# Performance work log

Measured on AMD Instinct MI355X. Metric: run time of the kernel, lower is better.

## Reference

```python
import jax, jax.numpy as jnp
import numpy as np

D_MODEL = 1024
N_STATE = 64
BASEWIDTH = 3
BC_SCALE = (D_MODEL / BASEWIDTH) ** -0.5  # 'mup' mode width_mult**-0.5
RMS_EPS = 1.1920928955078125e-07  # torch.finfo(float32).eps (RMSNorm eps=None default)


def setup_inputs() -> dict:
    key = jax.random.key(0)
    k1, k2, k3, k4 = jax.random.split(key, 4)
    Bsz, L = 4, 2048
    u = jax.random.normal(k1, (Bsz, D_MODEL, L), dtype=jnp.float32)
    A = jax.random.uniform(k2, (N_STATE,), dtype=jnp.float32) * 0.1  # buffer: rand(N)*A_scale
    B = (jax.random.normal(k3, (N_STATE, D_MODEL), dtype=jnp.float32) + 0.1) * BC_SCALE
    C = (jax.random.normal(k4, (N_STATE, D_MODEL), dtype=jnp.float32) + 0.1) * BC_SCALE
    D = jnp.ones((D_MODEL,), dtype=jnp.float32)
    norm_w = jnp.ones((D_MODEL,), dtype=jnp.float32)
    return {"L": L, "u": u, "A": A, "B": B, "C": C, "D": D, "norm_w": norm_w}


def _ssm(u, A, B, C, D, norm_w):
    # u: [b, d, l]
    scale = BC_SCALE  # applied to Bu, Cu in 'mup' hyperparam mode
    Bu = jnp.einsum('nd,bdl->bnl', B, u) * scale  # [b, n, l]
    Cu = jnp.einsum('nd,bdl->bnl', C, u) * scale  # [b, n, l]
    b, d, l = u.shape
    # shifted_delta == 1 (delta path commented out in source), so
    # h_{t} = A * h_{t-1} + Bu[:, :, t] (outer) u[:, :, t]
    h0 = jnp.zeros((b, d, A.shape[0]), dtype=u.dtype)

    def step(h, xs):
        bu_t, cu_t, u_t = xs  # [b,n], [b,n], [b,d]
        h = h * A + u_t[:, :, None] * bu_t[:, None, :]  # [b, d, n]
        y_t = jnp.einsum('bn,bdn->bd', cu_t, h)
        return h, y_t

    xs = (jnp.moveaxis(Bu, 2, 0), jnp.moveaxis(Cu, 2, 0), jnp.moveaxis(u, 2, 0))
    _, y = jax.lax.scan(step, h0, xs)  # y: [l, b, d]
    y = jnp.moveaxis(y, 0, 2).transpose(1, 0, 2) if False else jnp.transpose(y, (1, 2, 0))  # [b, d, l]
    out = y + u * D[None, :, None]
    # RMSNorm over d_model (apply in [b, l, d] layout)
    x = jnp.transpose(out, (0, 2, 1))  # [b, l, d]
    ms = jnp.mean(x * x, axis=-1, keepdims=True)
    x = x * jax.lax.rsqrt(ms + RMS_EPS) * norm_w
    return jnp.transpose(x, (0, 2, 1))  # [b, d, l]


def reference(L, u, A, B, C, D, norm_w):
    del L  # sequence length == u.shape[-1]
    return _ssm(u, A, B, C, D, norm_w)
```

## Files before the change

### kernel.cpp

```cpp
#include <hip/hip_runtime.h>
#include <stdint.h>

#define DM 1024
#define LS 2048
#define RMS_EPS 1.1920928955078125e-07f
#define S2 0.0029296875f

typedef __attribute__((ext_vector_type(8))) short bf16x8;
typedef __attribute__((ext_vector_type(4))) float f32x4;

__device__ __forceinline__ unsigned short f2bf(float f) {
  uint32_t u = __builtin_bit_cast(uint32_t, f);
  u += 0x7FFFu + ((u >> 16) & 1u);
  return (unsigned short)(u >> 16);
}

__global__ __launch_bounds__(256) void k0_prep(const float* __restrict__ B,
                                               const float* __restrict__ C,
                                               unsigned short* __restrict__ Bbf) {
  int i4 = blockIdx.x * 256 + threadIdx.x;
  const float4* src = (i4 < 16384) ? (const float4*)B : (const float4*)C;
  float4 v = src[i4 & 16383];
  ushort4 o;
  o.x = f2bf(v.x); o.y = f2bf(v.y); o.z = f2bf(v.z); o.w = f2bf(v.w);
  ((ushort4*)Bbf)[i4] = o;
}

__global__ __launch_bounds__(256) void k1_gemm(const float* __restrict__ u,
                                               const unsigned short* __restrict__ Bbf,
                                               float* __restrict__ BuCuT) {
  const int b    = blockIdx.y;
  const int l0   = blockIdx.x * 16;
  const int lane = threadIdx.x & 63;
  const int w    = threadIdx.x >> 6;
  const float* ub = u + (size_t)b * DM * LS;

  __shared__ bf16x8 tile[128][16];

  {
    const int lq = lane & 3;
    const int kg = lane >> 2;
    const int kbase = 256 * w + 16 * kg;
    #pragma unroll
    for (int h = 0; h < 2; ++h) {
      float4 vv[8];
      #pragma unroll
      for (int r = 0; r < 8; ++r)
        vv[r] = *(const float4*)(ub + (size_t)(kbase + 8*h + r) * LS + l0 + 4*lq);
      const int k8 = 32*w + 2*kg + h;
      #pragma unroll
      for (int c = 0; c < 4; ++c) {
        union { bf16x8 v; unsigned short s[8]; } t;
        #pragma unroll
        for (int r = 0; r < 8; ++r) t.s[r] = f2bf(((const float*)&vv[r])[c]);
        tile[k8][(4*lq + c) ^ (k8 & 3)] = t.v;
      }
    }
  }
  __syncthreads();

  const int n = lane & 15;
  const int q = lane >> 4;
  f32x4 acc[2] = {};
  #pragma unroll 4
  for (int it = 0; it < 32; ++it) {
    bf16x8 bfrag = tile[4*it + q][n ^ q];
    #pragma unroll
    for (int rt = 0; rt < 2; ++rt) {
      int row = 32*w + 16*rt + n;
      bf16x8 a = *(const bf16x8*)(Bbf + (size_t)row * DM + 32*it + 8*q);
      acc[rt] = __builtin_amdgcn_mfma_f32_16x16x32_bf16(a, bfrag, acc[rt], 0, 0, 0);
    }
  }

  float* ob = BuCuT + (size_t)b * LS * 128;
  #pragma unroll
  for (int rt = 0; rt < 2; ++rt) {
    int col = l0 + n;
    int row = 32*w + 16*rt + 4*q;
    *(f32x4*)(ob + (size_t)col * 128 + row) = acc[rt];
  }
}

__global__ __launch_bounds__(256) void k2_kw(const float* __restrict__ BuCuT,
                                             const float* __restrict__ A,
                                             float* __restrict__ Kw) {
  const int b  = blockIdx.y;
  const int t0 = blockIdx.x * 64;
  const int tl = threadIdx.x >> 2;
  const int p  = threadIdx.x & 3;
  const int t  = t0 + tl;
  const float* base = BuCuT + (size_t)b * LS * 128;

  float pw[16], aa[16];
  #pragma unroll
  for (int i = 0; i < 4; ++i) {
    float4 c4 = *(const float4*)(base + (size_t)t * 128 + 64 + 16*p + 4*i);
    float4 a4 = *(const float4*)(A + 16*p + 4*i);
    pw[4*i+0] = c4.x * S2; aa[4*i+0] = a4.x;
    pw[4*i+1] = c4.y * S2; aa[4*i+1] = a4.y;
    pw[4*i+2] = c4.z * S2; aa[4*i+2] = a4.z;
    pw[4*i+3] = c4.w * S2; aa[4*i+3] = a4.w;
  }
  float part[16];
  #pragma unroll
  for (int j = 0; j < 16; ++j) {
    float s = 0.f;
    if (t - j >= 0) {
      const float* bu = base + (size_t)(t - j) * 128 + 16*p;
      #pragma unroll
      for (int i = 0; i < 16; i += 4) {
        float4 b4 = *(const float4*)(bu + i);
        s = fmaf(pw[i+0], b4.x, s); s = fmaf(pw[i+1], b4.y, s);
        s = fmaf(pw[i+2], b4.z, s); s = fmaf(pw[i+3], b4.w, s);
      }
    }
    part[j] = s;
    #pragma unroll
    for (int i = 0; i < 16; ++i) pw[i] *= aa[i];
  }
  __shared__ float ss[64][68];
  #pragma unroll
  for (int j = 0; j < 16; ++j) ss[tl][p*17 + j] = part[j];
  __syncthreads();
  const int o  = threadIdx.x * 4;
  const int t2 = o >> 4;
  const int j0 = o & 15;
  float4 r;
  r.x = ss[t2][j0+0] + ss[t2][17+j0+0] + ss[t2][34+j0+0] + ss[t2][51+j0+0];
  r.y = ss[t2][j0+1] + ss[t2][17+j0+1] + ss[t2][34+j0+1] + ss[t2][51+j0+1];
  r.z = ss[t2][j0+2] + ss[t2][17+j0+2] + ss[t2][34+j0+2] + ss[t2][51+j0+2];
  r.w = ss[t2][j0+3] + ss[t2][17+j0+3] + ss[t2][34+j0+3] + ss[t2][51+j0+3];
  *(float4*)(Kw + ((size_t)b * LS + t0 + t2) * 16 + j0) = r;
}

__global__ __launch_bounds__(256) void k3_conv(const float* __restrict__ u,
                                               const float* __restrict__ Kw,
                                               const float* __restrict__ Dv,
                                               const float* __restrict__ nw,
                                               float* __restrict__ out) {
  const int b  = blockIdx.y;
  const int t0 = blockIdx.x * 16;
  const int tg = threadIdx.x & 3;
  const int dr = threadIdx.x >> 2;
  const float* ub = u + (size_t)b * DM * LS;
  float* ob = out + (size_t)b * DM * LS;

  float kw[4][16];
  #pragma unroll
  for (int k = 0; k < 4; ++k) {
    const float* kp = Kw + ((size_t)b * LS + t0 + 4*tg + k) * 16;
    #pragma unroll
    for (int i = 0; i < 4; ++i) {
      float4 v = *(const float4*)(kp + 4*i);
      kw[k][4*i+0] = v.x; kw[k][4*i+1] = v.y; kw[k][4*i+2] = v.z; kw[k][4*i+3] = v.w;
    }
  }

  const int cbase = t0 - 16 + 4*tg;
  float y[16][4];
  float ps[4] = {0.f, 0.f, 0.f, 0.f};
  #pragma unroll
  for (int c = 0; c < 16; ++c) {
    const int d = dr + 64*c;
    const float* row = ub + (size_t)d * LS;
    float wr[20];
    #pragma unroll
    for (int s5 = 0; s5 < 5; ++s5) {
      int g = cbase + 4*s5;
      float4 v;
      if (g >= 0) v = *(const float4*)(row + g);
      else        v = make_float4(0.f, 0.f, 0.f, 0.f);
      wr[4*s5+0] = v.x; wr[4*s5+1] = v.y; wr[4*s5+2] = v.z; wr[4*s5+3] = v.w;
    }
    const float Dd = Dv[d];
    #pragma unroll
    for (int k = 0; k < 4; ++k) {
      float acc = wr[16+k] * Dd;
      #pragma unroll
      for (int j = 0; j < 16; ++j)
        acc = fmaf(kw[k][j], wr[16 + k - j], acc);
      y[c][k] = acc;
      ps[k] = fmaf(acc, acc, ps[k]);
    }
  }

  __shared__ float ss[16][68];
  #pragma unroll
  for (int k = 0; k < 4; ++k) ss[4*tg + k][dr] = ps[k];
  __syncthreads();
  __shared__ float rsq[16];
  if (threadIdx.x < 16) {
    float s = 0.f;
    #pragma unroll
    for (int i = 0; i < 16; ++i) {
      float4 v = *(const float4*)&ss[threadIdx.x][4*i];
      s += (v.x + v.y) + (v.z + v.w);
    }
    rsq[threadIdx.x] = rsqrtf(s * (1.f/1024.f) + RMS_EPS);
  }
  __syncthreads();
  float rq[4];
  #pragma unroll
  for (int k = 0; k < 4; ++k) rq[k] = rsq[4*tg + k];
  #pragma unroll
  for (int c = 0; c < 16; ++c) {
    const int d = dr + 64*c;
    const float wn = nw[d];
    float4 o;
    o.x = y[c][0] * rq[0] * wn;
    o.y = y[c][1] * rq[1] * wn;
    o.z = y[c][2] * rq[2] * wn;
    o.w = y[c][3] * rq[3] * wn;
    *(float4*)(ob + (size_t)d * LS + t0 + 4*tg) = o;
  }
}

extern "C" void kernel_launch(void* const* d_in, const int* in_sizes, int n_in,
                              void* d_out, int out_size, void* d_ws, size_t ws_size,
                              hipStream_t stream) {
  const float* u  = (const float*)d_in[1];
  const float* A  = (const float*)d_in[2];
  const float* B  = (const float*)d_in[3];
  const float* C  = (const float*)d_in[4];
  const float* Dv = (const float*)d_in[5];
  const float* nw = (const float*)d_in[6];
  float* out = (float*)d_out;

  float* BuCuT = (float*)d_ws;
  float* Kw    = (float*)((char*)d_ws + (4u << 20));
  unsigned short* Bbf = (unsigned short*)((char*)d_ws + (4u << 20) + (512u << 10));

  k0_prep<<<dim3(128),    dim3(256), 0, stream>>>(B, C, Bbf);
  k1_gemm<<<dim3(128, 4), dim3(256), 0, stream>>>(u, Bbf, BuCuT);
  k2_kw  <<<dim3(32, 4),  dim3(256), 0, stream>>>(BuCuT, A, Kw);
  k3_conv<<<dim3(128, 4), dim3(256), 0, stream>>>(u, Kw, Dv, nw, out);
}
```

Before: 155.5 us.

## Pack conv kernel weights to bf16 and widen conv blocks to 512 threads

The per-timestep convolution weights written by k2 are now stored as packed bf16 pairs, which halves their footprint and the registers k3 needs to hold them. k3 moves to 512-thread blocks with 8 channel rows per thread instead of 16, cutting the per-thread y array in half to raise occupancy. k2 is reshaped to 128-thread blocks with twice as many blocks to spread work over more CUs. Rounding the kernel weights to bf16 adds precision loss to the output.

```diff
diff --git a/kernel.cpp b/kernel.cpp
--- a/kernel.cpp
+++ b/kernel.cpp
@@ -82,11 +82,11 @@
   }
 }
 
-__global__ __launch_bounds__(256) void k2_kw(const float* __restrict__ BuCuT,
+__global__ __launch_bounds__(128) void k2_kw(const float* __restrict__ BuCuT,
                                              const float* __restrict__ A,
-                                             float* __restrict__ Kw) {
+                                             uint32_t* __restrict__ Kwp) {
   const int b  = blockIdx.y;
-  const int t0 = blockIdx.x * 64;
+  const int t0 = blockIdx.x * 32;
   const int tl = threadIdx.x >> 2;
   const int p  = threadIdx.x & 3;
   const int t  = t0 + tl;
@@ -119,7 +119,7 @@
     #pragma unroll
     for (int i = 0; i < 16; ++i) pw[i] *= aa[i];
   }
-  __shared__ float ss[64][68];
+  __shared__ float ss[32][68];
   #pragma unroll
   for (int j = 0; j < 16; ++j) ss[tl][p*17 + j] = part[j];
   __syncthreads();
@@ -131,14 +131,17 @@
   r.y = ss[t2][j0+1] + ss[t2][17+j0+1] + ss[t2][34+j0+1] + ss[t2][51+j0+1];
   r.z = ss[t2][j0+2] + ss[t2][17+j0+2] + ss[t2][34+j0+2] + ss[t2][51+j0+2];
   r.w = ss[t2][j0+3] + ss[t2][17+j0+3] + ss[t2][34+j0+3] + ss[t2][51+j0+3];
-  *(float4*)(Kw + ((size_t)b * LS + t0 + t2) * 16 + j0) = r;
-}
-
-__global__ __launch_bounds__(256) void k3_conv(const float* __restrict__ u,
-                                               const float* __restrict__ Kw,
-                                               const float* __restrict__ Dv,
-                                               const float* __restrict__ nw,
-                                               float* __restrict__ out) {
+  uint2 pp;
+  pp.x = (uint32_t)f2bf(r.x) | ((uint32_t)f2bf(r.y) << 16);
+  pp.y = (uint32_t)f2bf(r.z) | ((uint32_t)f2bf(r.w) << 16);
+  *(uint2*)(Kwp + ((size_t)b * LS + t0 + t2) * 8 + (j0 >> 1)) = pp;
+}
+
+__global__ __launch_bounds__(512, 4) void k3_conv(const float* __restrict__ u,
+                                                  const uint32_t* __restrict__ Kwp,
+                                                  const float* __restrict__ Dv,
+                                                  const float* __restrict__ nw,
+                                                  float* __restrict__ out) {
   const int b  = blockIdx.y;
   const int t0 = blockIdx.x * 16;
   const int tg = threadIdx.x & 3;
@@ -146,46 +149,46 @@
   const float* ub = u + (size_t)b * DM * LS;
   float* ob = out + (size_t)b * DM * LS;
 
-  float kw[4][16];
+  uint32_t kwp[4][8];
   #pragma unroll
   for (int k = 0; k < 4; ++k) {
-    const float* kp = Kw + ((size_t)b * LS + t0 + 4*tg + k) * 16;
-    #pragma unroll
-    for (int i = 0; i < 4; ++i) {
-      float4 v = *(const float4*)(kp + 4*i);
-      kw[k][4*i+0] = v.x; kw[k][4*i+1] = v.y; kw[k][4*i+2] = v.z; kw[k][4*i+3] = v.w;
-    }
+    const uint32_t* kp = Kwp + ((size_t)b * LS + t0 + 4*tg + k) * 8;
+    *(uint4*)&kwp[k][0] = *(const uint4*)kp;
+    *(uint4*)&kwp[k][4] = *(const uint4*)(kp + 4);
   }
 
   const int cbase = t0 - 16 + 4*tg;
-  float y[16][4];
+  float y[8][4];
   float ps[4] = {0.f, 0.f, 0.f, 0.f};
   #pragma unroll
-  for (int c = 0; c < 16; ++c) {
-    const int d = dr + 64*c;
+  for (int c = 0; c < 8; ++c) {
+    const int d = dr + 128*c;
     const float* row = ub + (size_t)d * LS;
     float wr[20];
     #pragma unroll
     for (int s5 = 0; s5 < 5; ++s5) {
       int g = cbase + 4*s5;
-      float4 v;
-      if (g >= 0) v = *(const float4*)(row + g);
-      else        v = make_float4(0.f, 0.f, 0.f, 0.f);
+      float4 v = (g >= 0) ? *(const float4*)(row + g)
+                          : make_float4(0.f, 0.f, 0.f, 0.f);
       wr[4*s5+0] = v.x; wr[4*s5+1] = v.y; wr[4*s5+2] = v.z; wr[4*s5+3] = v.w;
     }
     const float Dd = Dv[d];
     #pragma unroll
     for (int k = 0; k < 4; ++k) {
-      float acc = wr[16+k] * Dd;
-      #pragma unroll
-      for (int j = 0; j < 16; ++j)
-        acc = fmaf(kw[k][j], wr[16 + k - j], acc);
+      float acc = wr[16 + k] * Dd;
+      #pragma unroll
+      for (int jp = 0; jp < 8; ++jp) {
+        float klo = __builtin_bit_cast(float, kwp[k][jp] << 16);
+        float khi = __builtin_bit_cast(float, kwp[k][jp] & 0xffff0000u);
+        acc = fmaf(klo, wr[16 + k - 2*jp], acc);
+        acc = fmaf(khi, wr[16 + k - 2*jp - 1], acc);
+      }
       y[c][k] = acc;
       ps[k] = fmaf(acc, acc, ps[k]);
     }
   }
 
-  __shared__ float ss[16][68];
+  __shared__ float ss[16][132];
   #pragma unroll
   for (int k = 0; k < 4; ++k) ss[4*tg + k][dr] = ps[k];
   __syncthreads();
@@ -193,7 +196,7 @@
   if (threadIdx.x < 16) {
     float s = 0.f;
     #pragma unroll
-    for (int i = 0; i < 16; ++i) {
+    for (int i = 0; i < 32; ++i) {
       float4 v = *(const float4*)&ss[threadIdx.x][4*i];
       s += (v.x + v.y) + (v.z + v.w);
     }
@@ -204,8 +207,8 @@
   #pragma unroll
   for (int k = 0; k < 4; ++k) rq[k] = rsq[4*tg + k];
   #pragma unroll
-  for (int c = 0; c < 16; ++c) {
-    const int d = dr + 64*c;
+  for (int c = 0; c < 8; ++c) {
+    const int d = dr + 128*c;
     const float wn = nw[d];
     float4 o;
     o.x = y[c][0] * rq[0] * wn;
@@ -227,12 +230,12 @@
   const float* nw = (const float*)d_in[6];
   float* out = (float*)d_out;
 
-  float* BuCuT = (float*)d_ws;
-  float* Kw    = (float*)((char*)d_ws + (4u << 20));
-  unsigned short* Bbf = (unsigned short*)((char*)d_ws + (4u << 20) + (512u << 10));
+  float*    BuCuT = (float*)d_ws;
+  uint32_t* Kwp   = (uint32_t*)((char*)d_ws + (4u << 20));
+  unsigned short* Bbf = (unsigned short*)((char*)d_ws + (4u << 20) + (256u << 10));
 
   k0_prep<<<dim3(128),    dim3(256), 0, stream>>>(B, C, Bbf);
   k1_gemm<<<dim3(128, 4), dim3(256), 0, stream>>>(u, Bbf, BuCuT);
-  k2_kw  <<<dim3(32, 4),  dim3(256), 0, stream>>>(BuCuT, A, Kw);
-  k3_conv<<<dim3(128, 4), dim3(256), 0, stream>>>(u, Kw, Dv, nw, out);
-}
+  k2_kw  <<<dim3(64, 4),  dim3(128), 0, stream>>>(BuCuT, A, Kwp);
+  k3_conv<<<dim3(128, 4), dim3(512), 0, stream>>>(u, Kwp, Dv, nw, out);
+}
```

New measurement: 298.6 us. 1.92x slower.
